# Kernel tuning notes

Hardware: AMD Instinct MI355X
Metric: run time of the kernel (lower is better)

The kernel has to match this reference:

```python
import jax, jax.numpy as jnp
import numpy as np

V, E, H, L = 32000, 512, 1024, 2
B, S = 16, 128


def _gru_cell(x, h, w_ih, w_hh, b_ih, b_hh):
    # PyTorch GRUCell: gates ordered (r, z, n), chunks of size H
    gi = x @ w_ih.T + b_ih            # (B, 3H)
    gh = h @ w_hh.T + b_hh            # (B, 3H)
    i_r, i_z, i_n = jnp.split(gi, 3, axis=-1)
    h_r, h_z, h_n = jnp.split(gh, 3, axis=-1)
    r = jax.nn.sigmoid(i_r + h_r)
    z = jax.nn.sigmoid(i_z + h_z)
    n = jnp.tanh(i_n + r * h_n)
    return (1.0 - z) * n + z * h


def setup_inputs() -> dict:
    key = jax.random.key(0)
    ks = jax.random.split(key, 16)
    s = lambda fan: 1.0 / np.sqrt(fan)
    inp = {
        "hidden": jax.random.normal(ks[0], (L, B, H), jnp.float32),
        "trg": jax.random.randint(ks[1], (B, S), 0, V),
        "embedding": jax.random.normal(ks[2], (V, E), jnp.float32) * 0.02,
        # layer 0 GRU (input_size=E)
        "w_ih0": jax.random.uniform(ks[3], (3 * H, E), jnp.float32, -s(H), s(H)),
        "w_hh0": jax.random.uniform(ks[4], (3 * H, H), jnp.float32, -s(H), s(H)),
        "b_ih0": jnp.zeros((3 * H,), jnp.float32),
        "b_hh0": jnp.zeros((3 * H,), jnp.float32),
        # layer 1 GRU (input_size=H)
        "w_ih1": jax.random.uniform(ks[5], (3 * H, H), jnp.float32, -s(H), s(H)),
        "w_hh1": jax.random.uniform(ks[6], (3 * H, H), jnp.float32, -s(H), s(H)),
        "b_ih1": jnp.zeros((3 * H,), jnp.float32),
        "b_hh1": jnp.zeros((3 * H,), jnp.float32),
        # output projection MLP: Linear(H,H) -> ReLU -> Linear(H,E)
        "w1": jax.random.uniform(ks[7], (H, H), jnp.float32, -s(H), s(H)),
        "b1": jnp.zeros((H,), jnp.float32),
        "w2": jax.random.uniform(ks[8], (E, H), jnp.float32, -s(H), s(H)),
        "b2": jnp.zeros((E,), jnp.float32),
        # generator bias (weight tied to embedding)
        "b_gen": jnp.zeros((V,), jnp.float32),
    }
    return inp


def reference(hidden, trg, embedding, w_ih0, w_hh0, b_ih0, b_hh0,
              w_ih1, w_hh1, b_ih1, b_hh1, w1, b1, w2, b2, b_gen):
    def step(h, tok):
        # h: (L, B, H); tok: (B,)
        x = embedding[tok]                                 # (B, E)
        h0 = _gru_cell(x, h[0], w_ih0, w_hh0, b_ih0, b_hh0)
        h1 = _gru_cell(h0, h[1], w_ih1, w_hh1, b_ih1, b_hh1)
        new_h = jnp.stack([h0, h1], axis=0)
        out = jax.nn.relu(h1 @ w1.T + b1) @ w2.T + b2      # (B, E)
        logit = out @ embedding.T + b_gen                  # (B, V) weight-tied
        return new_h, logit

    _, logits = jax.lax.scan(step, hidden, trg.T)          # (S, B, V)
    return jnp.transpose(logits, (1, 0, 2))                # (B, S, V)
```

## Files before the change

kernel.cpp:

```cpp
#include <hip/hip_runtime.h>
#include <math.h>

#define Sn 128
#define Bn 16
#define Hn 1024
#define En 512
#define Vn 32000
#define H3 3072
#define NL0 32
#define NL1 64

typedef _Float16 h16;
typedef __attribute__((ext_vector_type(4))) _Float16 h16x4;
typedef __attribute__((ext_vector_type(8))) _Float16 h16x8;
typedef __attribute__((ext_vector_type(4))) float f32x4;

#define Q_EMB   4096000
#define Q_WIH0  (Q_EMB + 393216)
#define Q_W1    (Q_WIH0 + 262144)
#define Q_W2    (Q_W1 + 131072)
#define Q_WHH0  (Q_W2 + 786432)
#define Q_WIH1  (Q_WHH0 + 786432)
#define Q_WHH1  (Q_WIH1 + 786432)
#define Q_HID   (Q_WHH1 + 8192)
__global__ __launch_bounds__(256) void cvt_all_k(
    const float* __restrict__ emb, const float* __restrict__ wih0,
    const float* __restrict__ w1, const float* __restrict__ w2,
    const float* __restrict__ whh0, const float* __restrict__ wih1,
    const float* __restrict__ whh1, const float* __restrict__ hid,
    h16* __restrict__ E, h16* __restrict__ A, h16* __restrict__ B1,
    h16* __restrict__ B2, h16* __restrict__ D0, h16* __restrict__ D1,
    h16* __restrict__ D2, h16* __restrict__ HD)
{
  int i = blockIdx.x * 256 + threadIdx.x;
  const float* s; h16* d; int o;
  if      (i < Q_EMB)  { s = emb;  d = E;  o = i; }
  else if (i < Q_WIH0) { s = wih0; d = A;  o = i - Q_EMB; }
  else if (i < Q_W1)   { s = w1;   d = B1; o = i - Q_WIH0; }
  else if (i < Q_W2)   { s = w2;   d = B2; o = i - Q_W1; }
  else if (i < Q_WHH0) { s = whh0; d = D0; o = i - Q_W2; }
  else if (i < Q_WIH1) { s = wih1; d = D1; o = i - Q_WHH0; }
  else if (i < Q_WHH1) { s = whh1; d = D2; o = i - Q_WIH1; }
  else                 { s = hid;  d = HD; o = i - Q_WHH1; }
  float4 v = *(const float4*)(s + (size_t)o * 4);
  h16x4 ov = { (h16)v.x, (h16)v.y, (h16)v.z, (h16)v.w };
  *(h16x4*)(d + (size_t)o * 4) = ov;
}

__global__ void embed_k(const int* __restrict__ trg, const float* __restrict__ emb,
                        h16* __restrict__ Xh) {
  int t = blockIdx.x;
  int s = t >> 4, b = t & 15;
  int tok = trg[b * Sn + s];
  const float* src = emb + (size_t)tok * En;
  int e = threadIdx.x * 4;
  float4 v = *(const float4*)(src + e);
  h16x4 o = { (h16)v.x, (h16)v.y, (h16)v.z, (h16)v.w };
  *(h16x4*)(Xh + (size_t)t * En + e) = o;
}

template<int OUT_MODE, bool RELU, bool SWZ>
__global__ __launch_bounds__(256) void gemm_bt(
    const h16* __restrict__ A, const h16* __restrict__ B,
    const float* __restrict__ bias, void* __restrict__ C,
    int M, int N, int K)
{
  __shared__ h16 As[128 * 64];
  __shared__ h16 Bs[128 * 64];
  int tid = threadIdx.x;
  int l = tid & 63, wv = tid >> 6;
  int wr = wv >> 1, wc = wv & 1;

  int work = blockIdx.x;
  if (SWZ) { int q = gridDim.x >> 3; work = (work & 7) * q + (work >> 3); }
  int nMp = M >> 7;
  int brow = (work % nMp) << 7;
  int bcol = (work / nMp) << 7;

  f32x4 acc[4][4];
#pragma unroll
  for (int m = 0; m < 4; ++m)
#pragma unroll
    for (int n = 0; n < 4; ++n) acc[m][n] = (f32x4){0.f, 0.f, 0.f, 0.f};

  int nkt = K >> 6;
  for (int kt = 0; kt < nkt; ++kt) {
    const h16* Ag = A + (size_t)brow * K + kt * 64;
    const h16* Bg = B + (size_t)bcol * K + kt * 64;
#pragma unroll
    for (int c = tid; c < 2048; c += 256) {
      int half = c >> 10;
      int cc = c & 1023;
      int row = cc >> 3, slot = cc & 7;
      const h16* src = (half ? Bg : Ag) + (size_t)row * K + slot * 8;
      uint4 v = *(const uint4*)src;
      h16* dst = (half ? Bs : As) + row * 64 + ((slot ^ (row & 7)) << 3);
      *(uint4*)dst = v;
    }
    __syncthreads();
#pragma unroll
    for (int kk = 0; kk < 2; ++kk) {
      h16x8 af[4], bfr[4];
      int rb = wr * 64 + (l & 15);
      int cb2 = wc * 64 + (l & 15);
      int slot = kk * 4 + (l >> 4);
#pragma unroll
      for (int m = 0; m < 4; ++m) {
        int r = rb + m * 16;
        af[m] = *(const h16x8*)&As[r * 64 + ((slot ^ (r & 7)) << 3)];
      }
#pragma unroll
      for (int n = 0; n < 4; ++n) {
        int r = cb2 + n * 16;
        bfr[n] = *(const h16x8*)&Bs[r * 64 + ((slot ^ (r & 7)) << 3)];
      }
#pragma unroll
      for (int m = 0; m < 4; ++m)
#pragma unroll
        for (int n = 0; n < 4; ++n)
          acc[m][n] = __builtin_amdgcn_mfma_f32_16x16x32_f16(af[m], bfr[n], acc[m][n], 0, 0, 0);
    }
    __syncthreads();
  }

#pragma unroll
  for (int m = 0; m < 4; ++m) {
    int row0 = brow + wr * 64 + m * 16 + ((l >> 4) << 2);
#pragma unroll
    for (int n = 0; n < 4; ++n) {
      int col = bcol + wc * 64 + n * 16 + (l & 15);
      float bv = bias ? bias[col] : 0.f;
#pragma unroll
      for (int i = 0; i < 4; ++i) {
        int row = row0 + i;
        float v = acc[m][n][i] + bv;
        if (RELU) v = fmaxf(v, 0.f);
        if (OUT_MODE == 1) {
          ((h16*)C)[(size_t)row * N + col] = (h16)v;
        } else if (OUT_MODE == 2) {
          int rr = ((row & 15) << 7) + (row >> 4);
          ((float*)C)[(size_t)rr * N + col] = v;
        } else {
          ((float*)C)[(size_t)row * N + col] = v;
        }
      }
    }
  }
}

__global__ __launch_bounds__(256, 1) void gemm_bt256(
    const h16* __restrict__ A, const h16* __restrict__ B,
    const float* __restrict__ bias, float* __restrict__ C,
    int M, int N, int K)
{
  __shared__ h16 As[128 * 64];
  __shared__ h16 Bs[256 * 64];
  int tid = threadIdx.x;
  int l = tid & 63, wv = tid >> 6;
  int wr = wv >> 1, wc = wv & 1;

  int work = blockIdx.x;
  int q = gridDim.x >> 3; work = (work & 7) * q + (work >> 3);
  int nMp = M >> 7;
  int brow = (work % nMp) << 7;
  int bcol = (work / nMp) << 8;

  f32x4 acc[4][8];
#pragma unroll
  for (int m = 0; m < 4; ++m)
#pragma unroll
    for (int n = 0; n < 8; ++n) acc[m][n] = (f32x4){0.f, 0.f, 0.f, 0.f};

  int nkt = K >> 6;
  for (int kt = 0; kt < nkt; ++kt) {
    const h16* Ag = A + (size_t)brow * K + kt * 64;
    const h16* Bg = B + (size_t)bcol * K + kt * 64;
#pragma unroll
    for (int c = tid; c < 3072; c += 256) {
      int isB = (c >= 1024);
      int cc = isB ? (c - 1024) : c;
      int row = cc >> 3, slot = cc & 7;
      const h16* src = (isB ? Bg : Ag) + (size_t)row * K + slot * 8;
      uint4 v = *(const uint4*)src;
      h16* dst = (isB ? Bs : As) + row * 64 + ((slot ^ (row & 7)) << 3);
      *(uint4*)dst = v;
    }
    __syncthreads();
#pragma unroll
    for (int kk = 0; kk < 2; ++kk) {
      h16x8 af[4], bfr[8];
      int rb = wr * 64 + (l & 15);
      int cb2 = wc * 128 + (l & 15);
      int slot = kk * 4 + (l >> 4);
#pragma unroll
      for (int m = 0; m < 4; ++m) {
        int r = rb + m * 16;
        af[m] = *(const h16x8*)&As[r * 64 + ((slot ^ (r & 7)) << 3)];
      }
#pragma unroll
      for (int n = 0; n < 8; ++n) {
        int r = cb2 + n * 16;
        bfr[n] = *(const h16x8*)&Bs[r * 64 + ((slot ^ (r & 7)) << 3)];
      }
#pragma unroll
      for (int m = 0; m < 4; ++m)
#pragma unroll
        for (int n = 0; n < 8; ++n)
          acc[m][n] = __builtin_amdgcn_mfma_f32_16x16x32_f16(af[m], bfr[n], acc[m][n], 0, 0, 0);
    }
    __syncthreads();
  }

#pragma unroll
  for (int m = 0; m < 4; ++m) {
    int row0 = brow + wr * 64 + m * 16 + ((l >> 4) << 2);
#pragma unroll
    for (int n = 0; n < 8; ++n) {
      int col = bcol + wc * 128 + n * 16 + (l & 15);
      float bv = bias[col];
#pragma unroll
      for (int i = 0; i < 4; ++i) {
        int row = row0 + i;
        int rr = ((row & 15) << 7) + (row >> 4);
        C[(size_t)rr * N + col] = acc[m][n][i] + bv;
      }
    }
  }
}

__global__ __launch_bounds__(384, 1) void gru_mfma(
    const float* __restrict__ gi0,
    const float* __restrict__ hidden,
    const h16* __restrict__ hinit16,
    const h16* __restrict__ whh0, const float* __restrict__ bhh0,
    const h16* __restrict__ wih1, const float* __restrict__ bih1,
    const h16* __restrict__ whh1, const float* __restrict__ bhh1,
    h16* __restrict__ h0ring,
    h16* __restrict__ H1A,
    int* __restrict__ flags)
{
  __shared__ float exch[5][256];
  int bid = blockIdx.x;
  int tid = threadIdx.x;
  int w = tid >> 6, l = tid & 63;
  int li = l & 15;
  int ko = (l >> 4) << 3;
  int b0 = (l >> 4) << 2;

  __threadfence();

  int* fL0 = flags;
  int* fL1 = flags + 1024;

  if (bid < NL0) {
    int gate = w >> 1, ch = w & 1;
    int j = bid * 32 + ch * 16 + li;
    h16x8 Bf[32];
    {
      const h16* wp = whh0 + ((size_t)((gate << 10) + j) << 10) + ko;
#pragma unroll
      for (int t = 0; t < 32; ++t) Bf[t] = *(const h16x8*)(wp + t * 32);
    }
    float bR = 0.f, bZ = 0.f, bN = 0.f;
    float hprev[4];
    if (gate == 2) {
      bR = bhh0[j]; bZ = bhh0[1024 + j]; bN = bhh0[2048 + j];
#pragma unroll
      for (int i = 0; i < 4; ++i) hprev[i] = hidden[((b0 + i) << 10) + j];
    }

    for (int s = 0; s < Sn; ++s) {
      if (s > 0) {
        if (w == 0 && l < NL0)
          while (__hip_atomic_load(&fL0[l << 5], __ATOMIC_RELAXED, __HIP_MEMORY_SCOPE_AGENT) < s) {}
        __syncthreads();
        asm volatile("" ::: "memory");
      }
      float gr[4], gz[4], gn[4];
      if (gate == 2) {
        const float* gb = gi0 + ((size_t)s << 4) * H3;
#pragma unroll
        for (int i = 0; i < 4; ++i) {
          const float* g = gb + (size_t)(b0 + i) * H3 + j;
          gr[i] = g[0]; gz[i] = g[1024]; gn[i] = g[2048];
        }
      }
      const h16* hsrc = (s == 0) ? hinit16 : h0ring + (((size_t)(s - 1)) << 14);
      const h16* Ap = hsrc + (li << 10) + ko;
      f32x4 acc = (f32x4){0.f, 0.f, 0.f, 0.f};
#pragma unroll
      for (int t = 0; t < 32; ++t)
        acc = __builtin_amdgcn_mfma_f32_16x16x32_f16(*(const h16x8*)(Ap + t * 32), Bf[t], acc, 0, 0, 0);
      if (w < 4) {
#pragma unroll
        for (int i = 0; i < 4; ++i) exch[w][((b0 + i) << 4) + li] = acc[i];
      }
      __syncthreads();
      if (gate == 2) {
#pragma unroll
        for (int i = 0; i < 4; ++i) {
          int e = ((b0 + i) << 4) + li;
          float r = 1.f / (1.f + expf(-(exch[ch][e] + bR + gr[i])));
          float z = 1.f / (1.f + expf(-(exch[2 + ch][e] + bZ + gz[i])));
          float n = tanhf(gn[i] + r * (acc[i] + bN));
          float out = (1.f - z) * n + z * hprev[i];
          hprev[i] = out;
          h16 hv = (h16)out; unsigned short us; __builtin_memcpy(&us, &hv, 2);
          __hip_atomic_store((unsigned short*)h0ring + (((size_t)s) << 14) + ((b0 + i) << 10) + j,
                             us, __ATOMIC_RELAXED, __HIP_MEMORY_SCOPE_AGENT);
        }
      }
      __syncthreads();
      if (tid == 0)
        __hip_atomic_store(&fL0[bid << 5], s + 1, __ATOMIC_RELAXED, __HIP_MEMORY_SCOPE_AGENT);
    }
  } else {
    int bl = bid - NL0;
    int j = (bl << 4) + li;
    int isHH = (w >= 3);
    int gate = isHH ? (w - 3) : w;
    h16x8 Bf[32];
    {
      const h16* wsrc = isHH ? whh1 : wih1;
      const h16* wp = wsrc + ((size_t)((gate << 10) + j) << 10) + ko;
#pragma unroll
      for (int t = 0; t < 32; ++t) Bf[t] = *(const h16x8*)(wp + t * 32);
    }
    float bIR = 0.f, bIZ = 0.f, bIN = 0.f, bHR = 0.f, bHZ = 0.f, bHN = 0.f;
    float hprev[4];
    if (w == 5) {
      bIR = bih1[j]; bIZ = bih1[1024 + j]; bIN = bih1[2048 + j];
      bHR = bhh1[j]; bHZ = bhh1[1024 + j]; bHN = bhh1[2048 + j];
#pragma unroll
      for (int i = 0; i < 4; ++i) hprev[i] = hidden[16384 + ((b0 + i) << 10) + j];
    }

    for (int s = 1; s <= Sn; ++s) {
      if (w == 0) {
        if (l < NL0)
          while (__hip_atomic_load(&fL0[l << 5], __ATOMIC_RELAXED, __HIP_MEMORY_SCOPE_AGENT) < s) {}
      } else if (w == 1 && s >= 2) {
        while (__hip_atomic_load(&fL1[l << 5], __ATOMIC_RELAXED, __HIP_MEMORY_SCOPE_AGENT) < s) {}
      }
      __syncthreads();
      asm volatile("" ::: "memory");
      const h16* hsrc = isHH
          ? ((s == 1) ? hinit16 + 16384 : H1A + (((size_t)(s - 2)) << 14))
          : (h0ring + (((size_t)(s - 1)) << 14));
      const h16* Ap = hsrc + (li << 10) + ko;
      f32x4 acc = (f32x4){0.f, 0.f, 0.f, 0.f};
#pragma unroll
      for (int t = 0; t < 32; ++t)
        acc = __builtin_amdgcn_mfma_f32_16x16x32_f16(*(const h16x8*)(Ap + t * 32), Bf[t], acc, 0, 0, 0);
      if (w < 5) {
#pragma unroll
        for (int i = 0; i < 4; ++i) exch[w][((b0 + i) << 4) + li] = acc[i];
      }
      __syncthreads();
      if (w == 5) {
#pragma unroll
        for (int i = 0; i < 4; ++i) {
          int e = ((b0 + i) << 4) + li;
          float r = 1.f / (1.f + expf(-(exch[0][e] + bIR + exch[3][e] + bHR)));
          float z = 1.f / (1.f + expf(-(exch[1][e] + bIZ + exch[4][e] + bHZ)));
          float n = tanhf(exch[2][e] + bIN + r * (acc[i] + bHN));
          float out = (1.f - z) * n + z * hprev[i];
          hprev[i] = out;
          h16 hv = (h16)out; unsigned short us; __builtin_memcpy(&us, &hv, 2);
          __hip_atomic_store((unsigned short*)H1A + (((size_t)(s - 1)) << 14) + ((b0 + i) << 10) + j,
                             us, __ATOMIC_RELAXED, __HIP_MEMORY_SCOPE_AGENT);
        }
      }
      __syncthreads();
      if (tid == 0)
        __hip_atomic_store(&fL1[bl << 5], s + 1, __ATOMIC_RELAXED, __HIP_MEMORY_SCOPE_AGENT);
    }
  }
}

extern "C" void kernel_launch(void* const* d_in, const int* in_sizes, int n_in,
                              void* d_out, int out_size, void* d_ws, size_t ws_size,
                              hipStream_t stream) {
  const float* hidden = (const float*)d_in[0];
  const int*   trg    = (const int*)d_in[1];
  const float* emb    = (const float*)d_in[2];
  const float* w_ih0  = (const float*)d_in[3];
  const float* w_hh0  = (const float*)d_in[4];
  const float* b_ih0  = (const float*)d_in[5];
  const float* b_hh0  = (const float*)d_in[6];
  const float* w_ih1  = (const float*)d_in[7];
  const float* w_hh1  = (const float*)d_in[8];
  const float* b_ih1  = (const float*)d_in[9];
  const float* b_hh1  = (const float*)d_in[10];
  const float* w1     = (const float*)d_in[11];
  const float* b1     = (const float*)d_in[12];
  const float* w2     = (const float*)d_in[13];
  const float* b2     = (const float*)d_in[14];
  const float* b_gen  = (const float*)d_in[15];

  char* ws = (char*)d_ws;
  size_t off = 0;
  float* GI0    = (float*)(ws + off); off += (size_t)Sn * Bn * H3 * 4;
  h16* Xh       = (h16*)(ws + off);   off += (size_t)Sn * Bn * En * 2;
  h16* embH     = (h16*)(ws + off);   off += (size_t)Vn * En * 2;
  h16* wih0H    = (h16*)(ws + off);   off += (size_t)H3 * En * 2;
  h16* w1H      = (h16*)(ws + off);   off += (size_t)Hn * Hn * 2;
  h16* w2H      = (h16*)(ws + off);   off += (size_t)En * Hn * 2;
  h16* whh0H    = (h16*)(ws + off);   off += (size_t)H3 * Hn * 2;
  h16* wih1H    = (h16*)(ws + off);   off += (size_t)H3 * Hn * 2;
  h16* whh1H    = (h16*)(ws + off);   off += (size_t)H3 * Hn * 2;
  h16* H1A      = (h16*)(ws + off);   off += (size_t)Sn * Bn * Hn * 2;
  h16* h0ring   = (h16*)(ws + off);   off += (size_t)Sn * Bn * Hn * 2;
  h16* hinit16  = (h16*)(ws + off);   off += (size_t)2 * Bn * Hn * 2;
  int* flags    = (int*)(ws + off);   off += 16384;
  h16* Tb = (h16*)GI0;
  h16* Ub = (h16*)((char*)GI0 + (8u << 20));

  cvt_all_k<<<28320, 256, 0, stream>>>(emb, w_ih0, w1, w2, w_hh0, w_ih1, w_hh1, hidden,
                                       embH, wih0H, w1H, w2H, whh0H, wih1H, whh1H, hinit16);
  embed_k<<<Sn * Bn, 128, 0, stream>>>(trg, emb, Xh);

  gemm_bt<0, false, true><<<384, 256, 0, stream>>>(Xh, wih0H, b_ih0, GI0, Sn * Bn, H3, En);

  (void)hipMemsetAsync(flags, 0, 16384, stream);
  gru_mfma<<<NL0 + NL1, 384, 0, stream>>>(GI0, hidden, hinit16,
                                          whh0H, b_hh0, wih1H, b_ih1, whh1H, b_hh1,
                                          h0ring, H1A, flags);

  gemm_bt<1, true,  true><<<128,  256, 0, stream>>>(H1A, w1H, b1, Tb, Sn * Bn, Hn, Hn);
  gemm_bt<1, false, true><<<64,   256, 0, stream>>>(Tb, w2H, b2, Ub, Sn * Bn, En, Hn);
  gemm_bt256<<<2000, 256, 0, stream>>>(Ub, embH, b_gen, (float*)d_out, Sn * Bn, Vn, En);
}
```

Measured before the change: 1.488 ms.

## Restructure persistent GRU kernel: LDS-staged weights and hidden states, 64+64 block split

Layer 0 now runs on 64 blocks instead of 32. Each block keeps its W_hh0 slice in LDS (about 128 KB of dynamic shared memory) rather than in registers. Every step, the previous hidden state is copied into swizzled LDS once per block and shared by all waves, and the MFMA chain is split across two accumulators. Layer 1 streams its weights from global memory in chunks instead of holding them in registers. Flags are packed tighter and signalled by the gate wave after a vmcnt wait, which removes a block barrier. The input-gate GEMM also writes a per-block tiled layout so gate loads are contiguous. The aim is to raise parallelism and cut redundant global reads of h on the sequential critical path, at the cost of LDS capacity and re-reading layer-1 weights every step.

```diff
diff --git a/kernel.cpp b/kernel.cpp
--- a/kernel.cpp
+++ b/kernel.cpp
@@ -7,8 +7,6 @@
 #define En 512
 #define Vn 32000
 #define H3 3072
-#define NL0 32
-#define NL1 64
 
 typedef _Float16 h16;
 typedef __attribute__((ext_vector_type(4))) _Float16 h16x4;
@@ -140,6 +138,10 @@
         } else if (OUT_MODE == 2) {
           int rr = ((row & 15) << 7) + (row >> 4);
           ((float*)C)[(size_t)rr * N + col] = v;
+        } else if (OUT_MODE == 3) {
+          size_t idx = (size_t)((col & 1023) >> 4) * 98304 + (size_t)(row >> 4) * 768
+                     + (size_t)(row & 15) * 48 + (col >> 10) * 16 + (col & 15);
+          ((float*)C)[idx] = v;
         } else {
           ((float*)C)[(size_t)row * N + col] = v;
         }
@@ -228,8 +230,8 @@
   }
 }
 
-__global__ __launch_bounds__(384, 1) void gru_mfma(
-    const float* __restrict__ gi0,
+__global__ __launch_bounds__(384, 1) void gru_lds(
+    const float* __restrict__ gi2,
     const float* __restrict__ hidden,
     const h16* __restrict__ hinit16,
     const h16* __restrict__ whh0, const float* __restrict__ bhh0,
@@ -239,141 +241,184 @@
     h16* __restrict__ H1A,
     int* __restrict__ flags)
 {
-  __shared__ float exch[5][256];
+  extern __shared__ char dyn[];
   int bid = blockIdx.x;
   int tid = threadIdx.x;
   int w = tid >> 6, l = tid & 63;
   int li = l & 15;
-  int ko = (l >> 4) << 3;
   int b0 = (l >> 4) << 2;
 
   __threadfence();
-
   int* fL0 = flags;
-  int* fL1 = flags + 1024;
-
-  if (bid < NL0) {
-    int gate = w >> 1, ch = w & 1;
-    int j = bid * 32 + ch * 16 + li;
-    h16x8 Bf[32];
-    {
-      const h16* wp = whh0 + ((size_t)((gate << 10) + j) << 10) + ko;
-#pragma unroll
-      for (int t = 0; t < 32; ++t) Bf[t] = *(const h16x8*)(wp + t * 32);
-    }
-    float bR = 0.f, bZ = 0.f, bN = 0.f;
+  int* fL1 = flags + 512;
+
+  if (bid < 64) {
+    h16* Wlds = (h16*)dyn;
+    h16* sA   = (h16*)(dyn + 98304);
+    float* exch = (float*)(dyn + 131072);
+    int blk = bid, jb = blk << 4;
+
+    for (int i = tid; i < 6144; i += 384) {
+      int g = i >> 11, rem = i & 2047, t = rem >> 6, ll = rem & 63;
+      const h16* src = whh0 + ((size_t)((g << 10) + jb + (ll & 15)) << 10)
+                     + t * 32 + ((ll >> 4) << 3);
+      *(h16x8*)(Wlds + g * 16384 + t * 512 + ll * 8) = *(const h16x8*)src;
+    }
+    float bN = 0.f, bR = 0.f, bZ = 0.f;
     float hprev[4];
-    if (gate == 2) {
-      bR = bhh0[j]; bZ = bhh0[1024 + j]; bN = bhh0[2048 + j];
-#pragma unroll
-      for (int i = 0; i < 4; ++i) hprev[i] = hidden[((b0 + i) << 10) + j];
+    if (w == 2) {
+      bR = bhh0[jb + li]; bZ = bhh0[1024 + jb + li]; bN = bhh0[2048 + jb + li];
+#pragma unroll
+      for (int i = 0; i < 4; ++i) hprev[i] = hidden[((b0 + i) << 10) + jb + li];
     }
 
     for (int s = 0; s < Sn; ++s) {
-      if (s > 0) {
-        if (w == 0 && l < NL0)
-          while (__hip_atomic_load(&fL0[l << 5], __ATOMIC_RELAXED, __HIP_MEMORY_SCOPE_AGENT) < s) {}
-        __syncthreads();
-        asm volatile("" ::: "memory");
-      }
       float gr[4], gz[4], gn[4];
-      if (gate == 2) {
-        const float* gb = gi0 + ((size_t)s << 4) * H3;
+      if (w == 2) {
+        const float* gb = gi2 + (size_t)blk * 98304 + (size_t)s * 768;
 #pragma unroll
         for (int i = 0; i < 4; ++i) {
-          const float* g = gb + (size_t)(b0 + i) * H3 + j;
-          gr[i] = g[0]; gz[i] = g[1024]; gn[i] = g[2048];
-        }
-      }
+          gr[i] = gb[(b0 + i) * 48 + li];
+          gz[i] = gb[(b0 + i) * 48 + 16 + li];
+          gn[i] = gb[(b0 + i) * 48 + 32 + li];
+        }
+      }
+      if (s > 0 && w == 0) {
+        while (__hip_atomic_load(&fL0[l << 2], __ATOMIC_RELAXED, __HIP_MEMORY_SCOPE_AGENT) < s) {}
+      }
+      __syncthreads();
+      asm volatile("" ::: "memory");
       const h16* hsrc = (s == 0) ? hinit16 : h0ring + (((size_t)(s - 1)) << 14);
-      const h16* Ap = hsrc + (li << 10) + ko;
+#pragma unroll
+      for (int i = tid; i < 2048; i += 384) {
+        int r = i >> 7, g = i & 127;
+        h16x8 v = *(const h16x8*)(hsrc + r * 1024 + g * 8);
+        *(h16x8*)(sA + r * 1024 + ((g ^ (r & 7)) << 3)) = v;
+      }
+      __syncthreads();
       f32x4 acc = (f32x4){0.f, 0.f, 0.f, 0.f};
-#pragma unroll
-      for (int t = 0; t < 32; ++t)
-        acc = __builtin_amdgcn_mfma_f32_16x16x32_f16(*(const h16x8*)(Ap + t * 32), Bf[t], acc, 0, 0, 0);
-      if (w < 4) {
-#pragma unroll
-        for (int i = 0; i < 4; ++i) exch[w][((b0 + i) << 4) + li] = acc[i];
-      }
-      __syncthreads();
-      if (gate == 2) {
+      if (w < 3) {
+        const h16* wb = Wlds + w * 16384 + l * 8;
+        int r = li;
+        f32x4 a0 = (f32x4){0.f, 0.f, 0.f, 0.f};
+        f32x4 a1 = (f32x4){0.f, 0.f, 0.f, 0.f};
+#pragma unroll
+        for (int t = 0; t < 32; t += 2) {
+          int g0 = t * 4 + (l >> 4), g1 = (t + 1) * 4 + (l >> 4);
+          h16x8 A0 = *(const h16x8*)(sA + r * 1024 + ((g0 ^ (r & 7)) << 3));
+          h16x8 A1 = *(const h16x8*)(sA + r * 1024 + ((g1 ^ (r & 7)) << 3));
+          h16x8 B0 = *(const h16x8*)(wb + t * 512);
+          h16x8 B1v = *(const h16x8*)(wb + (t + 1) * 512);
+          a0 = __builtin_amdgcn_mfma_f32_16x16x32_f16(A0, B0, a0, 0, 0, 0);
+          a1 = __builtin_amdgcn_mfma_f32_16x16x32_f16(A1, B1v, a1, 0, 0, 0);
+        }
+        acc = a0 + a1;
+        if (w < 2) {
+#pragma unroll
+          for (int i = 0; i < 4; ++i) exch[w * 256 + ((b0 + i) << 4) + li] = acc[i];
+        }
+      }
+      __syncthreads();
+      if (w == 2) {
 #pragma unroll
         for (int i = 0; i < 4; ++i) {
           int e = ((b0 + i) << 4) + li;
-          float r = 1.f / (1.f + expf(-(exch[ch][e] + bR + gr[i])));
-          float z = 1.f / (1.f + expf(-(exch[2 + ch][e] + bZ + gz[i])));
+          float r = 1.f / (1.f + expf(-(exch[e] + bR + gr[i])));
+          float z = 1.f / (1.f + expf(-(exch[256 + e] + bZ + gz[i])));
           float n = tanhf(gn[i] + r * (acc[i] + bN));
           float out = (1.f - z) * n + z * hprev[i];
           hprev[i] = out;
           h16 hv = (h16)out; unsigned short us; __builtin_memcpy(&us, &hv, 2);
-          __hip_atomic_store((unsigned short*)h0ring + (((size_t)s) << 14) + ((b0 + i) << 10) + j,
+          __hip_atomic_store((unsigned short*)h0ring + (((size_t)s) << 14) + ((b0 + i) << 10) + jb + li,
                              us, __ATOMIC_RELAXED, __HIP_MEMORY_SCOPE_AGENT);
         }
-      }
-      __syncthreads();
-      if (tid == 0)
-        __hip_atomic_store(&fL0[bid << 5], s + 1, __ATOMIC_RELAXED, __HIP_MEMORY_SCOPE_AGENT);
+        asm volatile("s_waitcnt vmcnt(0)" ::: "memory");
+        if (l == 0)
+          __hip_atomic_store(&fL0[blk << 2], s + 1, __ATOMIC_RELAXED, __HIP_MEMORY_SCOPE_AGENT);
+      }
     }
   } else {
-    int bl = bid - NL0;
-    int j = (bl << 4) + li;
+    h16* sA0 = (h16*)dyn;
+    h16* sA1 = (h16*)(dyn + 32768);
+    float* exch = (float*)(dyn + 65536);
+    int blk = bid - 64, jb = blk << 4;
     int isHH = (w >= 3);
     int gate = isHH ? (w - 3) : w;
-    h16x8 Bf[32];
-    {
-      const h16* wsrc = isHH ? whh1 : wih1;
-      const h16* wp = wsrc + ((size_t)((gate << 10) + j) << 10) + ko;
-#pragma unroll
-      for (int t = 0; t < 32; ++t) Bf[t] = *(const h16x8*)(wp + t * 32);
-    }
+    const h16* wsrc = isHH ? whh1 : wih1;
+    const h16* wp = wsrc + ((size_t)((gate << 10) + jb + li) << 10) + ((l >> 4) << 3);
+
     float bIR = 0.f, bIZ = 0.f, bIN = 0.f, bHR = 0.f, bHZ = 0.f, bHN = 0.f;
     float hprev[4];
     if (w == 5) {
-      bIR = bih1[j]; bIZ = bih1[1024 + j]; bIN = bih1[2048 + j];
-      bHR = bhh1[j]; bHZ = bhh1[1024 + j]; bHN = bhh1[2048 + j];
-#pragma unroll
-      for (int i = 0; i < 4; ++i) hprev[i] = hidden[16384 + ((b0 + i) << 10) + j];
+      bIR = bih1[jb + li]; bIZ = bih1[1024 + jb + li]; bIN = bih1[2048 + jb + li];
+      bHR = bhh1[jb + li]; bHZ = bhh1[1024 + jb + li]; bHN = bhh1[2048 + jb + li];
+#pragma unroll
+      for (int i = 0; i < 4; ++i) hprev[i] = hidden[16384 + ((b0 + i) << 10) + jb + li];
     }
 
     for (int s = 1; s <= Sn; ++s) {
       if (w == 0) {
-        if (l < NL0)
-          while (__hip_atomic_load(&fL0[l << 5], __ATOMIC_RELAXED, __HIP_MEMORY_SCOPE_AGENT) < s) {}
+        while (__hip_atomic_load(&fL0[l << 2], __ATOMIC_RELAXED, __HIP_MEMORY_SCOPE_AGENT) < s) {}
       } else if (w == 1 && s >= 2) {
-        while (__hip_atomic_load(&fL1[l << 5], __ATOMIC_RELAXED, __HIP_MEMORY_SCOPE_AGENT) < s) {}
+        while (__hip_atomic_load(&fL1[l << 2], __ATOMIC_RELAXED, __HIP_MEMORY_SCOPE_AGENT) < s - 1) {}
       }
       __syncthreads();
       asm volatile("" ::: "memory");
-      const h16* hsrc = isHH
-          ? ((s == 1) ? hinit16 + 16384 : H1A + (((size_t)(s - 2)) << 14))
-          : (h0ring + (((size_t)(s - 1)) << 14));
-      const h16* Ap = hsrc + (li << 10) + ko;
-      f32x4 acc = (f32x4){0.f, 0.f, 0.f, 0.f};
-#pragma unroll
-      for (int t = 0; t < 32; ++t)
-        acc = __builtin_amdgcn_mfma_f32_16x16x32_f16(*(const h16x8*)(Ap + t * 32), Bf[t], acc, 0, 0, 0);
+      const h16* src0 = h0ring + (((size_t)(s - 1)) << 14);
+      const h16* src1 = (s == 1) ? hinit16 + 16384 : H1A + (((size_t)(s - 2)) << 14);
+#pragma unroll
+      for (int i = tid; i < 4096; i += 384) {
+        int half = i >> 11, ii = i & 2047;
+        int r = ii >> 7, g = ii & 127;
+        const h16* sp = half ? src1 : src0;
+        h16* dp = half ? sA1 : sA0;
+        h16x8 v = *(const h16x8*)(sp + r * 1024 + g * 8);
+        *(h16x8*)(dp + r * 1024 + ((g ^ (r & 7)) << 3)) = v;
+      }
+      __syncthreads();
+      const h16* sA = isHH ? sA1 : sA0;
+      int r = li;
+      f32x4 a0 = (f32x4){0.f, 0.f, 0.f, 0.f};
+      f32x4 a1 = (f32x4){0.f, 0.f, 0.f, 0.f};
+#pragma unroll
+      for (int tb = 0; tb < 4; ++tb) {
+        h16x8 Bv[8], Av[8];
+#pragma unroll
+        for (int t = 0; t < 8; ++t) Bv[t] = *(const h16x8*)(wp + (tb * 8 + t) * 32);
+#pragma unroll
+        for (int t = 0; t < 8; ++t) {
+          int g = (tb * 8 + t) * 4 + (l >> 4);
+          Av[t] = *(const h16x8*)(sA + r * 1024 + ((g ^ (r & 7)) << 3));
+        }
+#pragma unroll
+        for (int t = 0; t < 8; t += 2) {
+          a0 = __builtin_amdgcn_mfma_f32_16x16x32_f16(Av[t], Bv[t], a0, 0, 0, 0);
+          a1 = __builtin_amdgcn_mfma_f32_16x16x32_f16(Av[t + 1], Bv[t + 1], a1, 0, 0, 0);
+        }
+      }
+      f32x4 acc = a0 + a1;
       if (w < 5) {
 #pragma unroll
-        for (int i = 0; i < 4; ++i) exch[w][((b0 + i) << 4) + li] = acc[i];
+        for (int i = 0; i < 4; ++i) exch[w * 256 + ((b0 + i) << 4) + li] = acc[i];
       }
       __syncthreads();
       if (w == 5) {
 #pragma unroll
         for (int i = 0; i < 4; ++i) {
           int e = ((b0 + i) << 4) + li;
-          float r = 1.f / (1.f + expf(-(exch[0][e] + bIR + exch[3][e] + bHR)));
-          float z = 1.f / (1.f + expf(-(exch[1][e] + bIZ + exch[4][e] + bHZ)));
-          float n = tanhf(exch[2][e] + bIN + r * (acc[i] + bHN));
-          float out = (1.f - z) * n + z * hprev[i];
+          float rr = 1.f / (1.f + expf(-(exch[e] + bIR + exch[768 + e] + bHR)));
+          float zz = 1.f / (1.f + expf(-(exch[256 + e] + bIZ + exch[1024 + e] + bHZ)));
+          float nn = tanhf(exch[512 + e] + bIN + rr * (acc[i] + bHN));
+          float out = (1.f - zz) * nn + zz * hprev[i];
           hprev[i] = out;
           h16 hv = (h16)out; unsigned short us; __builtin_memcpy(&us, &hv, 2);
-          __hip_atomic_store((unsigned short*)H1A + (((size_t)(s - 1)) << 14) + ((b0 + i) << 10) + j,
+          __hip_atomic_store((unsigned short*)H1A + (((size_t)(s - 1)) << 14) + ((b0 + i) << 10) + jb + li,
                              us, __ATOMIC_RELAXED, __HIP_MEMORY_SCOPE_AGENT);
         }
-      }
-      __syncthreads();
-      if (tid == 0)
-        __hip_atomic_store(&fL1[bl << 5], s + 1, __ATOMIC_RELAXED, __HIP_MEMORY_SCOPE_AGENT);
+        asm volatile("s_waitcnt vmcnt(0)" ::: "memory");
+        if (l == 0)
+          __hip_atomic_store(&fL1[blk << 2], s, __ATOMIC_RELAXED, __HIP_MEMORY_SCOPE_AGENT);
+      }
     }
   }
 }
@@ -400,7 +445,7 @@
 
   char* ws = (char*)d_ws;
   size_t off = 0;
-  float* GI0    = (float*)(ws + off); off += (size_t)Sn * Bn * H3 * 4;
+  float* GI2    = (float*)(ws + off); off += (size_t)64 * 128 * 768 * 4;
   h16* Xh       = (h16*)(ws + off);   off += (size_t)Sn * Bn * En * 2;
   h16* embH     = (h16*)(ws + off);   off += (size_t)Vn * En * 2;
   h16* wih0H    = (h16*)(ws + off);   off += (size_t)H3 * En * 2;
@@ -412,20 +457,23 @@
   h16* H1A      = (h16*)(ws + off);   off += (size_t)Sn * Bn * Hn * 2;
   h16* h0ring   = (h16*)(ws + off);   off += (size_t)Sn * Bn * Hn * 2;
   h16* hinit16  = (h16*)(ws + off);   off += (size_t)2 * Bn * Hn * 2;
-  int* flags    = (int*)(ws + off);   off += 16384;
-  h16* Tb = (h16*)GI0;
-  h16* Ub = (h16*)((char*)GI0 + (8u << 20));
+  int* flags    = (int*)(ws + off);   off += 8192;
+  h16* Tb = (h16*)GI2;
+  h16* Ub = (h16*)((char*)GI2 + (8u << 20));
 
   cvt_all_k<<<28320, 256, 0, stream>>>(emb, w_ih0, w1, w2, w_hh0, w_ih1, w_hh1, hidden,
                                        embH, wih0H, w1H, w2H, whh0H, wih1H, whh1H, hinit16);
   embed_k<<<Sn * Bn, 128, 0, stream>>>(trg, emb, Xh);
 
-  gemm_bt<0, false, true><<<384, 256, 0, stream>>>(Xh, wih0H, b_ih0, GI0, Sn * Bn, H3, En);
-
-  (void)hipMemsetAsync(flags, 0, 16384, stream);
-  gru_mfma<<<NL0 + NL1, 384, 0, stream>>>(GI0, hidden, hinit16,
-                                          whh0H, b_hh0, wih1H, b_ih1, whh1H, b_hh1,
-                                          h0ring, H1A, flags);
+  gemm_bt<3, false, true><<<384, 256, 0, stream>>>(Xh, wih0H, b_ih0, GI2, Sn * Bn, H3, En);
+
+  (void)hipMemsetAsync(flags, 0, 8192, stream);
+  const int LDSZ = 133120;
+  (void)hipFuncSetAttribute(reinterpret_cast<const void*>(gru_lds),
+                            hipFuncAttributeMaxDynamicSharedMemorySize, LDSZ);
+  gru_lds<<<128, 384, LDSZ, stream>>>(GI2, hidden, hinit16,
+                                      whh0H, b_hh0, wih1H, b_ih1, whh1H, b_hh1,
+                                      h0ring, H1A, flags);
 
   gemm_bt<1, true,  true><<<128,  256, 0, stream>>>(H1A, w1H, b1, Tb, Sn * Bn, Hn, Hn);
   gemm_bt<1, false, true><<<64,   256, 0, stream>>>(Tb, w2H, b2, Ub, Sn * Bn, En, Hn);
```

Result: slower. 2.006 ms (+34.7%).

## Rework GRU cross-block flag sync: packed flags, per-wave signaling, split MFMA chains

Applied to the files above, without the earlier changes.

The persistent GRU kernel's inter-block synchronization is restructured. Flags are packed contiguously instead of one per 128-byte line. Layer-0 blocks now signal per gate-n wave (two flags per block), with a waitcnt before the flag store instead of a block barrier. All 64 lanes of the polling wave spin with s_sleep, and the gi0 loads are issued before the wait. The MFMA dot product is split into two independent accumulator chains to shorten the dependency latency on the serial critical path. Packing the flags puts several of them in one cache line, which can add contention while blocks poll.

```diff
diff --git a/kernel.cpp b/kernel.cpp
--- a/kernel.cpp
+++ b/kernel.cpp
@@ -228,7 +228,7 @@
   }
 }
 
-__global__ __launch_bounds__(384, 1) void gru_mfma(
+__global__ __launch_bounds__(384) void gru_mfma2(
     const float* __restrict__ gi0,
     const float* __restrict__ hidden,
     const h16* __restrict__ hinit16,
@@ -250,7 +250,7 @@
   __threadfence();
 
   int* fL0 = flags;
-  int* fL1 = flags + 1024;
+  int* fL1 = flags + 64;
 
   if (bid < NL0) {
     int gate = w >> 1, ch = w & 1;
@@ -270,12 +270,6 @@
     }
 
     for (int s = 0; s < Sn; ++s) {
-      if (s > 0) {
-        if (w == 0 && l < NL0)
-          while (__hip_atomic_load(&fL0[l << 5], __ATOMIC_RELAXED, __HIP_MEMORY_SCOPE_AGENT) < s) {}
-        __syncthreads();
-        asm volatile("" ::: "memory");
-      }
       float gr[4], gz[4], gn[4];
       if (gate == 2) {
         const float* gb = gi0 + ((size_t)s << 4) * H3;
@@ -285,12 +279,22 @@
           gr[i] = g[0]; gz[i] = g[1024]; gn[i] = g[2048];
         }
       }
+      if (s > 0 && w == 0) {
+        while (__hip_atomic_load(&fL0[l], __ATOMIC_RELAXED, __HIP_MEMORY_SCOPE_AGENT) < s)
+          __builtin_amdgcn_s_sleep(1);
+      }
+      __syncthreads();
+      asm volatile("" ::: "memory");
       const h16* hsrc = (s == 0) ? hinit16 : h0ring + (((size_t)(s - 1)) << 14);
       const h16* Ap = hsrc + (li << 10) + ko;
-      f32x4 acc = (f32x4){0.f, 0.f, 0.f, 0.f};
-#pragma unroll
-      for (int t = 0; t < 32; ++t)
-        acc = __builtin_amdgcn_mfma_f32_16x16x32_f16(*(const h16x8*)(Ap + t * 32), Bf[t], acc, 0, 0, 0);
+      f32x4 a0 = (f32x4){0.f, 0.f, 0.f, 0.f};
+      f32x4 a1 = (f32x4){0.f, 0.f, 0.f, 0.f};
+#pragma unroll
+      for (int t = 0; t < 32; t += 2) {
+        a0 = __builtin_amdgcn_mfma_f32_16x16x32_f16(*(const h16x8*)(Ap + t * 32), Bf[t], a0, 0, 0, 0);
+        a1 = __builtin_amdgcn_mfma_f32_16x16x32_f16(*(const h16x8*)(Ap + (t + 1) * 32), Bf[t + 1], a1, 0, 0, 0);
+      }
+      f32x4 acc = a0 + a1;
       if (w < 4) {
 #pragma unroll
         for (int i = 0; i < 4; ++i) exch[w][((b0 + i) << 4) + li] = acc[i];
@@ -309,14 +313,14 @@
           __hip_atomic_store((unsigned short*)h0ring + (((size_t)s) << 14) + ((b0 + i) << 10) + j,
                              us, __ATOMIC_RELAXED, __HIP_MEMORY_SCOPE_AGENT);
         }
-      }
-      __syncthreads();
-      if (tid == 0)
-        __hip_atomic_store(&fL0[bid << 5], s + 1, __ATOMIC_RELAXED, __HIP_MEMORY_SCOPE_AGENT);
+        asm volatile("s_waitcnt vmcnt(0)" ::: "memory");
+        if (l == 0)
+          __hip_atomic_store(&fL0[bid * 2 + ch], s + 1, __ATOMIC_RELAXED, __HIP_MEMORY_SCOPE_AGENT);
+      }
     }
   } else {
-    int bl = bid - NL0;
-    int j = (bl << 4) + li;
+    int idx = bid - NL0;
+    int j = (idx << 4) + li;
     int isHH = (w >= 3);
     int gate = isHH ? (w - 3) : w;
     h16x8 Bf[32];
@@ -337,10 +341,11 @@
 
     for (int s = 1; s <= Sn; ++s) {
       if (w == 0) {
-        if (l < NL0)
-          while (__hip_atomic_load(&fL0[l << 5], __ATOMIC_RELAXED, __HIP_MEMORY_SCOPE_AGENT) < s) {}
-      } else if (w == 1 && s >= 2) {
-        while (__hip_atomic_load(&fL1[l << 5], __ATOMIC_RELAXED, __HIP_MEMORY_SCOPE_AGENT) < s) {}
+        while (__hip_atomic_load(&fL0[l], __ATOMIC_RELAXED, __HIP_MEMORY_SCOPE_AGENT) < s)
+          __builtin_amdgcn_s_sleep(1);
+      } else if (w == 3 && s >= 2) {
+        while (__hip_atomic_load(&fL1[l], __ATOMIC_RELAXED, __HIP_MEMORY_SCOPE_AGENT) < s - 1)
+          __builtin_amdgcn_s_sleep(1);
       }
       __syncthreads();
       asm volatile("" ::: "memory");
@@ -348,10 +353,14 @@
           ? ((s == 1) ? hinit16 + 16384 : H1A + (((size_t)(s - 2)) << 14))
           : (h0ring + (((size_t)(s - 1)) << 14));
       const h16* Ap = hsrc + (li << 10) + ko;
-      f32x4 acc = (f32x4){0.f, 0.f, 0.f, 0.f};
-#pragma unroll
-      for (int t = 0; t < 32; ++t)
-        acc = __builtin_amdgcn_mfma_f32_16x16x32_f16(*(const h16x8*)(Ap + t * 32), Bf[t], acc, 0, 0, 0);
+      f32x4 a0 = (f32x4){0.f, 0.f, 0.f, 0.f};
+      f32x4 a1 = (f32x4){0.f, 0.f, 0.f, 0.f};
+#pragma unroll
+      for (int t = 0; t < 32; t += 2) {
+        a0 = __builtin_amdgcn_mfma_f32_16x16x32_f16(*(const h16x8*)(Ap + t * 32), Bf[t], a0, 0, 0, 0);
+        a1 = __builtin_amdgcn_mfma_f32_16x16x32_f16(*(const h16x8*)(Ap + (t + 1) * 32), Bf[t + 1], a1, 0, 0, 0);
+      }
+      f32x4 acc = a0 + a1;
       if (w < 5) {
 #pragma unroll
         for (int i = 0; i < 4; ++i) exch[w][((b0 + i) << 4) + li] = acc[i];
@@ -370,10 +379,10 @@
           __hip_atomic_store((unsigned short*)H1A + (((size_t)(s - 1)) << 14) + ((b0 + i) << 10) + j,
                              us, __ATOMIC_RELAXED, __HIP_MEMORY_SCOPE_AGENT);
         }
-      }
-      __syncthreads();
-      if (tid == 0)
-        __hip_atomic_store(&fL1[bl << 5], s + 1, __ATOMIC_RELAXED, __HIP_MEMORY_SCOPE_AGENT);
+        asm volatile("s_waitcnt vmcnt(0)" ::: "memory");
+        if (l == 0)
+          __hip_atomic_store(&fL1[idx], s, __ATOMIC_RELAXED, __HIP_MEMORY_SCOPE_AGENT);
+      }
     }
   }
 }
@@ -412,7 +421,7 @@
   h16* H1A      = (h16*)(ws + off);   off += (size_t)Sn * Bn * Hn * 2;
   h16* h0ring   = (h16*)(ws + off);   off += (size_t)Sn * Bn * Hn * 2;
   h16* hinit16  = (h16*)(ws + off);   off += (size_t)2 * Bn * Hn * 2;
-  int* flags    = (int*)(ws + off);   off += 16384;
+  int* flags    = (int*)(ws + off);   off += 4096;
   h16* Tb = (h16*)GI0;
   h16* Ub = (h16*)((char*)GI0 + (8u << 20));
 
@@ -422,10 +431,10 @@
 
   gemm_bt<0, false, true><<<384, 256, 0, stream>>>(Xh, wih0H, b_ih0, GI0, Sn * Bn, H3, En);
 
-  (void)hipMemsetAsync(flags, 0, 16384, stream);
-  gru_mfma<<<NL0 + NL1, 384, 0, stream>>>(GI0, hidden, hinit16,
-                                          whh0H, b_hh0, wih1H, b_ih1, whh1H, b_hh1,
-                                          h0ring, H1A, flags);
+  (void)hipMemsetAsync(flags, 0, 4096, stream);
+  gru_mfma2<<<NL0 + NL1, 384, 0, stream>>>(GI0, hidden, hinit16,
+                                           whh0H, b_hh0, wih1H, b_ih1, whh1H, b_hh1,
+                                           h0ring, H1A, flags);
 
   gemm_bt<1, true,  true><<<128,  256, 0, stream>>>(H1A, w1H, b1, Tb, Sn * Bn, Hn, Hn);
   gemm_bt<1, false, true><<<64,   256, 0, stream>>>(Tb, w2H, b2, Ub, Sn * Bn, En, Hn);
```

New measurement: 1.863 ms. 1.25x slower.
